# Performance work log

Hardware: AMD Instinct MI355X
Metric: run time of the kernel (lower is better)

The kernel has to match this reference:

```python
import jax, jax.numpy as jnp
import numpy as np

N = 10000
IN_F = 512
OUT_F = 64
ALPHA = 0.2
NEG_INF = -9e15


def setup_inputs() -> dict:
    key = jax.random.key(0)
    k1, k2, k3, k4, k5, k6 = jax.random.split(key, 6)
    x = jax.random.normal(k1, (N, IN_F), dtype=jnp.float32)
    adj = jax.random.randint(k2, (N, N), 0, 2).astype(jnp.float32)
    M = jax.random.uniform(k3, (N, N), dtype=jnp.float32)
    W = jax.random.normal(k4, (IN_F, OUT_F), dtype=jnp.float32) * (1.414 / np.sqrt(IN_F))
    a_self = jax.random.normal(k5, (OUT_F, 1), dtype=jnp.float32) * 0.1
    a_neighs = jax.random.normal(k6, (OUT_F, 1), dtype=jnp.float32) * 0.1
    return {"x": x, "adj": adj, "M": M, "W": W, "a_self": a_self, "a_neighs": a_neighs}


def reference(x, adj, M, W, a_self, a_neighs):
    # h: [N, out_features]
    h = x @ W
    attn_for_self = h @ a_self      # [N, 1]
    attn_for_neighs = h @ a_neighs  # [N, 1]
    # outer-sum broadcast -> [N, N]
    attn_dense = attn_for_self + attn_for_neighs.T
    attn_dense = attn_dense * M
    attn_dense = jax.nn.leaky_relu(attn_dense, negative_slope=ALPHA)
    scores = jnp.where(adj > 0, attn_dense, NEG_INF)
    attention = jax.nn.softmax(scores, axis=1)
    h_prime = attention @ h  # [N, out_features]
    return jax.nn.elu(h_prime)  # concat=True path
```

## Files before the change

### kernel.cpp

```cpp
#include <hip/hip_runtime.h>
#include <math.h>

#define Nn 10000
#define NPAD 10048
#define INF_ 512
#define OUTF 64
#define ALPHA 0.2f
#define LOG2E 1.4426950408889634f

#define TI 32
#define TJ 64
#define NTILES ((Nn + TJ - 1) / TJ)
#define YS 6
#define TPC ((NTILES + YS - 1) / YS)

typedef __attribute__((ext_vector_type(8))) short bfrag;
typedef __attribute__((ext_vector_type(4))) float facc;

#define WS_S    0
#define WS_T    (Nn)
#define WS_TMAX (2*Nn)
#define WS_DEN  (2*Nn + 16)
#define WS_HP   (WS_DEN + YS*Nn)
#define WS_HBT  (WS_HP + YS*Nn*OUTF)

__device__ __forceinline__ unsigned short f2bf(float f) {
    unsigned int u = __float_as_uint(f);
    u += 0x7fffu + ((u >> 16) & 1u);
    return (unsigned short)(u >> 16);
}
__device__ __forceinline__ unsigned int pk2(float a, float b) {
    return (unsigned int)f2bf(a) | ((unsigned int)f2bf(b) << 16);
}

__global__ __launch_bounds__(256) void hgemm_kernel(
    const float* __restrict__ x, const float* __restrict__ W,
    const float* __restrict__ a_self, const float* __restrict__ a_neighs,
    unsigned short* __restrict__ hbfT, float* __restrict__ s, float* __restrict__ t)
{
    const int col  = threadIdx.x & 63;
    const int wid  = threadIdx.x >> 6;
    const int row0 = blockIdx.x * 16 + wid * 4;
    const float* x0 = x + row0 * INF_;

    float acc0 = 0.f, acc1 = 0.f, acc2 = 0.f, acc3 = 0.f;
    #pragma unroll 4
    for (int k4 = 0; k4 < INF_ / 4; ++k4) {
        const int k = k4 << 2;
        const float w0 = W[(k    ) * OUTF + col];
        const float w1 = W[(k + 1) * OUTF + col];
        const float w2 = W[(k + 2) * OUTF + col];
        const float w3 = W[(k + 3) * OUTF + col];
        const float4 xa = *(const float4*)(x0 +          k);
        const float4 xb = *(const float4*)(x0 +   INF_ + k);
        const float4 xc = *(const float4*)(x0 + 2*INF_ + k);
        const float4 xd = *(const float4*)(x0 + 3*INF_ + k);
        acc0 = fmaf(xa.x,w0, fmaf(xa.y,w1, fmaf(xa.z,w2, fmaf(xa.w,w3, acc0))));
        acc1 = fmaf(xb.x,w0, fmaf(xb.y,w1, fmaf(xb.z,w2, fmaf(xb.w,w3, acc1))));
        acc2 = fmaf(xc.x,w0, fmaf(xc.y,w1, fmaf(xc.z,w2, fmaf(xc.w,w3, acc2))));
        acc3 = fmaf(xd.x,w0, fmaf(xd.y,w1, fmaf(xd.z,w2, fmaf(xd.w,w3, acc3))));
    }
    ushort4 hb;
    hb.x = f2bf(acc0); hb.y = f2bf(acc1); hb.z = f2bf(acc2); hb.w = f2bf(acc3);
    *(ushort4*)(hbfT + (size_t)col * NPAD + row0) = hb;

    const float as = a_self[col], an = a_neighs[col];
    #define RED(ACC, U) { \
        float vs = (ACC) * as, vn = (ACC) * an; \
        _Pragma("unroll") \
        for (int d_ = 32; d_; d_ >>= 1) { vs += __shfl_xor(vs, d_); vn += __shfl_xor(vn, d_); } \
        if (col == 0) { s[row0 + (U)] = vs; t[row0 + (U)] = vn; } }
    RED(acc0, 0) RED(acc1, 1) RED(acc2, 2) RED(acc3, 3)
    #undef RED
}

__global__ __launch_bounds__(1024) void tmax_kernel(
    const float* __restrict__ t, float* __restrict__ tmax)
{
    __shared__ float red[16];
    float m = -3e38f;
    for (int i = threadIdx.x; i < Nn; i += 1024) m = fmaxf(m, t[i]);
    #pragma unroll
    for (int d = 32; d; d >>= 1) m = fmaxf(m, __shfl_xor(m, d));
    if ((threadIdx.x & 63) == 0) red[threadIdx.x >> 6] = m;
    __syncthreads();
    if (threadIdx.x < 16) {
        m = red[threadIdx.x];
        #pragma unroll
        for (int d = 8; d; d >>= 1) m = fmaxf(m, __shfl_xor(m, d));
        if (threadIdx.x == 0) *tmax = m;
    }
}

__global__ __launch_bounds__(256, 4) void gat_main_kernel(
    const float* __restrict__ adj, const float* __restrict__ Mm,
    const unsigned short* __restrict__ hbfT, const float* __restrict__ sv,
    const float* __restrict__ tv, const float* __restrict__ tmaxp,
    float* __restrict__ den_part, float* __restrict__ hp_part)
{
    __shared__ __align__(16) unsigned short hTl[OUTF][TJ + 8];
    __shared__ __align__(16) unsigned short Pl[TI][TJ + 8];

    const int tid = threadIdx.x;
    const int i0  = blockIdx.x * TI;
    const int tlo = blockIdx.y * TPC;
    const int thi = min(NTILES, tlo + TPC);

    const int rr = tid >> 3, jc = tid & 7;
    const int prow = i0 + rr;
    const bool rowok = prow < Nn;
    const float si = rowok ? sv[prow] : 0.0f;
    const float mc = fmaxf(0.0f, si + *tmaxp) * LOG2E;
    const float* aRow = adj + (size_t)prow * Nn;
    const float* mRow = Mm  + (size_t)prow * Nn;

    const int hc_ = tid >> 2, hseg = tid & 3;
    const unsigned short* hsrc = hbfT + (size_t)hc_ * NPAD + hseg * 16;

    const int lane = tid & 63, wv = tid >> 6;
    const int l15 = lane & 15, kq = lane >> 4;
    const int rb = wv & 1, cbp = wv >> 1;
    const unsigned short* aP  = &Pl[rb * 16 + l15][kq * 8];
    const unsigned short* bP0 = &hTl[cbp * 32 + l15][kq * 8];
    const unsigned short* bP1 = bP0 + 16 * (TJ + 8);

    facc accA = {0.f, 0.f, 0.f, 0.f}, accB = {0.f, 0.f, 0.f, 0.f};
    float denacc = 0.0f;

    const float4 z4 = make_float4(0.f, 0.f, 0.f, 0.f);
    float4 pa0 = z4, pa1 = z4, pm0 = z4, pm1 = z4, pt0 = z4, pt1 = z4;
    uint4 ph0 = make_uint4(0,0,0,0), ph1 = make_uint4(0,0,0,0);

    auto prefetch = [&](int tile) {
        const int j0 = tile * TJ;
        ph0 = *(const uint4*)(hsrc + j0);
        ph1 = *(const uint4*)(hsrc + j0 + 8);
        const int jl = j0 + (jc << 3);
        if (rowok && jl + 7 < Nn) {
            pa0 = *(const float4*)(aRow + jl); pa1 = *(const float4*)(aRow + jl + 4);
            pm0 = *(const float4*)(mRow + jl); pm1 = *(const float4*)(mRow + jl + 4);
            pt0 = *(const float4*)(tv   + jl); pt1 = *(const float4*)(tv   + jl + 4);
        } else {
            pa0 = pa1 = pm0 = pm1 = pt0 = pt1 = z4;
            if (rowok) {
                #define LD1(dst, base, off) if ((jl + (off)) < Nn) dst = (base)[jl + (off)]
                LD1(pa0.x, aRow, 0); LD1(pa0.y, aRow, 1); LD1(pa0.z, aRow, 2); LD1(pa0.w, aRow, 3);
                LD1(pa1.x, aRow, 4); LD1(pa1.y, aRow, 5); LD1(pa1.z, aRow, 6); LD1(pa1.w, aRow, 7);
                LD1(pm0.x, mRow, 0); LD1(pm0.y, mRow, 1); LD1(pm0.z, mRow, 2); LD1(pm0.w, mRow, 3);
                LD1(pm1.x, mRow, 4); LD1(pm1.y, mRow, 5); LD1(pm1.z, mRow, 6); LD1(pm1.w, mRow, 7);
                LD1(pt0.x, tv,   0); LD1(pt0.y, tv,   1); LD1(pt0.z, tv,   2); LD1(pt0.w, tv,   3);
                LD1(pt1.x, tv,   4); LD1(pt1.y, tv,   5); LD1(pt1.z, tv,   6); LD1(pt1.w, tv,   7);
                #undef LD1
            }
        }
    };

    #define PC(dst, av, mv, tvv) { \
        float e_ = (si + (tvv)) * (mv); \
        float l_ = fmaxf(e_, ALPHA * e_); \
        dst = ((av) > 0.0f) ? exp2f(fmaf(l_, LOG2E, -mc)) : 0.0f; }

    prefetch(tlo);
    for (int tile = tlo; tile < thi; ++tile) {
        __syncthreads();

        *(uint4*)&hTl[hc_][hseg * 16]     = ph0;
        *(uint4*)&hTl[hc_][hseg * 16 + 8] = ph1;

        float4 p40, p41;
        PC(p40.x, pa0.x, pm0.x, pt0.x); PC(p40.y, pa0.y, pm0.y, pt0.y);
        PC(p40.z, pa0.z, pm0.z, pt0.z); PC(p40.w, pa0.w, pm0.w, pt0.w);
        PC(p41.x, pa1.x, pm1.x, pt1.x); PC(p41.y, pa1.y, pm1.y, pt1.y);
        PC(p41.z, pa1.z, pm1.z, pt1.z); PC(p41.w, pa1.w, pm1.w, pt1.w);
        denacc += ((p40.x + p40.y) + (p40.z + p40.w)) + ((p41.x + p41.y) + (p41.z + p41.w));

        uint4 pw;
        pw.x = pk2(p40.x, p40.y); pw.y = pk2(p40.z, p40.w);
        pw.z = pk2(p41.x, p41.y); pw.w = pk2(p41.z, p41.w);
        *(uint4*)&Pl[rr][jc << 3] = pw;

        __syncthreads();

        if (tile + 1 < thi) prefetch(tile + 1);
        asm volatile("" ::: "memory");

        #pragma unroll
        for (int k0 = 0; k0 < TJ; k0 += 32) {
            const bfrag af = *(const bfrag*)(aP  + k0);
            const bfrag b0 = *(const bfrag*)(bP0 + k0);
            const bfrag b1 = *(const bfrag*)(bP1 + k0);
            accA = __builtin_amdgcn_mfma_f32_16x16x32_bf16(af, b0, accA, 0, 0, 0);
            accB = __builtin_amdgcn_mfma_f32_16x16x32_bf16(af, b1, accB, 0, 0, 0);
        }
    }
    #undef PC

    float d = denacc;
    d += __shfl_xor(d, 1); d += __shfl_xor(d, 2); d += __shfl_xor(d, 4);
    if (rowok && jc == 0) den_part[blockIdx.y * Nn + prow] = d;

    float* hp = hp_part + (size_t)blockIdx.y * (Nn * OUTF);
    const int orow = i0 + rb * 16 + (kq << 2);
    const int oc   = cbp * 32 + l15;
    #pragma unroll
    for (int r = 0; r < 4; ++r) {
        if (orow + r < Nn) {
            hp[(orow + r) * OUTF + oc]      = accA[r];
            hp[(orow + r) * OUTF + oc + 16] = accB[r];
        }
    }
}

__global__ __launch_bounds__(256) void finalize_kernel(
    const float* __restrict__ dp, const float* __restrict__ hp,
    float* __restrict__ out)
{
    const int idx = blockIdx.x * 256 + threadIdx.x;
    const int S = Nn * OUTF;
    const int row = idx >> 6;
    float num = 0.0f, den = 0.0f;
    #pragma unroll
    for (int y = 0; y < YS; ++y) {
        num += hp[(size_t)y * S + idx];
        den += dp[y * Nn + row];
    }
    const float v = num / den;
    out[idx] = (v > 0.0f) ? v : expm1f(v);
}

extern "C" void kernel_launch(void* const* d_in, const int* in_sizes, int n_in,
                              void* d_out, int out_size, void* d_ws, size_t ws_size,
                              hipStream_t stream) {
    const float* x        = (const float*)d_in[0];
    const float* adj      = (const float*)d_in[1];
    const float* Mm       = (const float*)d_in[2];
    const float* W        = (const float*)d_in[3];
    const float* a_self   = (const float*)d_in[4];
    const float* a_neighs = (const float*)d_in[5];

    float* out  = (float*)d_out;
    float* ws   = (float*)d_ws;
    float* s    = ws + WS_S;
    float* t    = ws + WS_T;
    float* tmax = ws + WS_TMAX;
    float* denp = ws + WS_DEN;
    float* hpp  = ws + WS_HP;
    unsigned short* hbfT = (unsigned short*)(ws + WS_HBT);

    hgemm_kernel<<<Nn / 16, 256, 0, stream>>>(x, W, a_self, a_neighs, hbfT, s, t);
    tmax_kernel<<<1, 1024, 0, stream>>>(t, tmax);
    gat_main_kernel<<<dim3((Nn + TI - 1) / TI, YS), 256, 0, stream>>>(
        adj, Mm, hbfT, s, t, tmax, denp, hpp);
    finalize_kernel<<<(Nn * OUTF) / 256, 256, 0, stream>>>(denp, hpp, out);
}
```

Before: 266.5 us.

## Compute attention weights directly in MFMA A-fragment registers, dropping LDS staging

The main kernel is restructured so each wave owns 16 rows and each lane loads adj/M values laid out to match the MFMA A-operand fragment. Probabilities are packed to bf16 straight into registers, and the B operand (transposed bf16 h) is read directly from global/L2. This removes the shared-memory tiles, both __syncthreads per tile, and the explicit software prefetch. Adj/M loads become nontemporal and TI grows to 64, so each wave computes all 64 output columns. The trade-offs are redundant per-wave global reads of h, loss of explicit load/compute overlap, and strided 32-byte row accesses per lane.

```diff
diff --git a/kernel.cpp b/kernel.cpp
--- a/kernel.cpp
+++ b/kernel.cpp
@@ -8,14 +8,16 @@
 #define ALPHA 0.2f
 #define LOG2E 1.4426950408889634f
 
-#define TI 32
+#define TI 64
 #define TJ 64
 #define NTILES ((Nn + TJ - 1) / TJ)
+#define NIB    ((Nn + TI - 1) / TI)
 #define YS 6
 #define TPC ((NTILES + YS - 1) / YS)
 
 typedef __attribute__((ext_vector_type(8))) short bfrag;
 typedef __attribute__((ext_vector_type(4))) float facc;
+typedef __attribute__((ext_vector_type(4))) float f32x4;
 
 #define WS_S    0
 #define WS_T    (Nn)
@@ -92,121 +94,119 @@
     }
 }
 
-__global__ __launch_bounds__(256, 4) void gat_main_kernel(
+__global__ __launch_bounds__(256) void gat_main_kernel(
     const float* __restrict__ adj, const float* __restrict__ Mm,
     const unsigned short* __restrict__ hbfT, const float* __restrict__ sv,
     const float* __restrict__ tv, const float* __restrict__ tmaxp,
     float* __restrict__ den_part, float* __restrict__ hp_part)
 {
-    __shared__ __align__(16) unsigned short hTl[OUTF][TJ + 8];
-    __shared__ __align__(16) unsigned short Pl[TI][TJ + 8];
-
-    const int tid = threadIdx.x;
-    const int i0  = blockIdx.x * TI;
-    const int tlo = blockIdx.y * TPC;
-    const int thi = min(NTILES, tlo + TPC);
-
-    const int rr = tid >> 3, jc = tid & 7;
-    const int prow = i0 + rr;
-    const bool rowok = prow < Nn;
-    const float si = rowok ? sv[prow] : 0.0f;
+    const int tid  = threadIdx.x;
+    const int lane = tid & 63, wv = tid >> 6;
+    const int l15  = lane & 15, kq = lane >> 4;
+    const int i0   = blockIdx.x * TI;
+    const int tlo  = blockIdx.y * TPC;
+    const int thi  = min(NTILES, tlo + TPC);
+
+    const int  row   = i0 + wv * 16 + l15;
+    const bool rowok = row < Nn;
+    const int  rowc  = min(row, Nn - 1);
+    const float si = sv[rowc];
     const float mc = fmaxf(0.0f, si + *tmaxp) * LOG2E;
-    const float* aRow = adj + (size_t)prow * Nn;
-    const float* mRow = Mm  + (size_t)prow * Nn;
-
-    const int hc_ = tid >> 2, hseg = tid & 3;
-    const unsigned short* hsrc = hbfT + (size_t)hc_ * NPAD + hseg * 16;
-
-    const int lane = tid & 63, wv = tid >> 6;
-    const int l15 = lane & 15, kq = lane >> 4;
-    const int rb = wv & 1, cbp = wv >> 1;
-    const unsigned short* aP  = &Pl[rb * 16 + l15][kq * 8];
-    const unsigned short* bP0 = &hTl[cbp * 32 + l15][kq * 8];
-    const unsigned short* bP1 = bP0 + 16 * (TJ + 8);
-
-    facc accA = {0.f, 0.f, 0.f, 0.f}, accB = {0.f, 0.f, 0.f, 0.f};
+    const float* aRow = adj + (size_t)rowc * Nn;
+    const float* mRow = Mm  + (size_t)rowc * Nn;
+
+    const unsigned short* hB0 = hbfT + (size_t)(l15     ) * NPAD;
+    const unsigned short* hB1 = hbfT + (size_t)(l15 + 16) * NPAD;
+    const unsigned short* hB2 = hbfT + (size_t)(l15 + 32) * NPAD;
+    const unsigned short* hB3 = hbfT + (size_t)(l15 + 48) * NPAD;
+
+    facc acc0 = {0.f,0.f,0.f,0.f}, acc1 = {0.f,0.f,0.f,0.f};
+    facc acc2 = {0.f,0.f,0.f,0.f}, acc3 = {0.f,0.f,0.f,0.f};
     float denacc = 0.0f;
-
-    const float4 z4 = make_float4(0.f, 0.f, 0.f, 0.f);
-    float4 pa0 = z4, pa1 = z4, pm0 = z4, pm1 = z4, pt0 = z4, pt1 = z4;
-    uint4 ph0 = make_uint4(0,0,0,0), ph1 = make_uint4(0,0,0,0);
-
-    auto prefetch = [&](int tile) {
-        const int j0 = tile * TJ;
-        ph0 = *(const uint4*)(hsrc + j0);
-        ph1 = *(const uint4*)(hsrc + j0 + 8);
-        const int jl = j0 + (jc << 3);
-        if (rowok && jl + 7 < Nn) {
-            pa0 = *(const float4*)(aRow + jl); pa1 = *(const float4*)(aRow + jl + 4);
-            pm0 = *(const float4*)(mRow + jl); pm1 = *(const float4*)(mRow + jl + 4);
-            pt0 = *(const float4*)(tv   + jl); pt1 = *(const float4*)(tv   + jl + 4);
-        } else {
-            pa0 = pa1 = pm0 = pm1 = pt0 = pt1 = z4;
-            if (rowok) {
-                #define LD1(dst, base, off) if ((jl + (off)) < Nn) dst = (base)[jl + (off)]
-                LD1(pa0.x, aRow, 0); LD1(pa0.y, aRow, 1); LD1(pa0.z, aRow, 2); LD1(pa0.w, aRow, 3);
-                LD1(pa1.x, aRow, 4); LD1(pa1.y, aRow, 5); LD1(pa1.z, aRow, 6); LD1(pa1.w, aRow, 7);
-                LD1(pm0.x, mRow, 0); LD1(pm0.y, mRow, 1); LD1(pm0.z, mRow, 2); LD1(pm0.w, mRow, 3);
-                LD1(pm1.x, mRow, 4); LD1(pm1.y, mRow, 5); LD1(pm1.z, mRow, 6); LD1(pm1.w, mRow, 7);
-                LD1(pt0.x, tv,   0); LD1(pt0.y, tv,   1); LD1(pt0.z, tv,   2); LD1(pt0.w, tv,   3);
-                LD1(pt1.x, tv,   4); LD1(pt1.y, tv,   5); LD1(pt1.z, tv,   6); LD1(pt1.w, tv,   7);
-                #undef LD1
-            }
-        }
-    };
 
     #define PC(dst, av, mv, tvv) { \
         float e_ = (si + (tvv)) * (mv); \
         float l_ = fmaxf(e_, ALPHA * e_); \
         dst = ((av) > 0.0f) ? exp2f(fmaf(l_, LOG2E, -mc)) : 0.0f; }
 
-    prefetch(tlo);
-    for (int tile = tlo; tile < thi; ++tile) {
-        __syncthreads();
-
-        *(uint4*)&hTl[hc_][hseg * 16]     = ph0;
-        *(uint4*)&hTl[hc_][hseg * 16 + 8] = ph1;
-
-        float4 p40, p41;
-        PC(p40.x, pa0.x, pm0.x, pt0.x); PC(p40.y, pa0.y, pm0.y, pt0.y);
-        PC(p40.z, pa0.z, pm0.z, pt0.z); PC(p40.w, pa0.w, pm0.w, pt0.w);
-        PC(p41.x, pa1.x, pm1.x, pt1.x); PC(p41.y, pa1.y, pm1.y, pt1.y);
-        PC(p41.z, pa1.z, pm1.z, pt1.z); PC(p41.w, pa1.w, pm1.w, pt1.w);
-        denacc += ((p40.x + p40.y) + (p40.z + p40.w)) + ((p41.x + p41.y) + (p41.z + p41.w));
-
-        uint4 pw;
-        pw.x = pk2(p40.x, p40.y); pw.y = pk2(p40.z, p40.w);
-        pw.z = pk2(p41.x, p41.y); pw.w = pk2(p41.z, p41.w);
-        *(uint4*)&Pl[rr][jc << 3] = pw;
-
-        __syncthreads();
-
-        if (tile + 1 < thi) prefetch(tile + 1);
-        asm volatile("" ::: "memory");
-
-        #pragma unroll
-        for (int k0 = 0; k0 < TJ; k0 += 32) {
-            const bfrag af = *(const bfrag*)(aP  + k0);
-            const bfrag b0 = *(const bfrag*)(bP0 + k0);
-            const bfrag b1 = *(const bfrag*)(bP1 + k0);
-            accA = __builtin_amdgcn_mfma_f32_16x16x32_bf16(af, b0, accA, 0, 0, 0);
-            accB = __builtin_amdgcn_mfma_f32_16x16x32_bf16(af, b1, accB, 0, 0, 0);
-        }
+    for (int t = tlo; t < thi; ++t) {
+        const int j0 = t * TJ;
+        const int jA = j0 + kq * 8;
+        const int jB = jA + 32;
+        const bool okA = jA < Nn, okB = jB < Nn;
+        const int  cA  = okA ? jA : (Nn - 8);
+        const int  cB  = okB ? jB : (Nn - 8);
+
+        const f32x4 a0 = __builtin_nontemporal_load((const f32x4*)(aRow + cA));
+        const f32x4 a1 = __builtin_nontemporal_load((const f32x4*)(aRow + cA + 4));
+        const f32x4 a2 = __builtin_nontemporal_load((const f32x4*)(aRow + cB));
+        const f32x4 a3 = __builtin_nontemporal_load((const f32x4*)(aRow + cB + 4));
+        const f32x4 m0 = __builtin_nontemporal_load((const f32x4*)(mRow + cA));
+        const f32x4 m1 = __builtin_nontemporal_load((const f32x4*)(mRow + cA + 4));
+        const f32x4 m2 = __builtin_nontemporal_load((const f32x4*)(mRow + cB));
+        const f32x4 m3 = __builtin_nontemporal_load((const f32x4*)(mRow + cB + 4));
+        const f32x4 t0 = *(const f32x4*)(tv + cA);
+        const f32x4 t1 = *(const f32x4*)(tv + cA + 4);
+        const f32x4 t2 = *(const f32x4*)(tv + cB);
+        const f32x4 t3 = *(const f32x4*)(tv + cB + 4);
+
+        f32x4 p0, p1, p2, p3;
+        PC(p0.x, a0.x, m0.x, t0.x); PC(p0.y, a0.y, m0.y, t0.y);
+        PC(p0.z, a0.z, m0.z, t0.z); PC(p0.w, a0.w, m0.w, t0.w);
+        PC(p1.x, a1.x, m1.x, t1.x); PC(p1.y, a1.y, m1.y, t1.y);
+        PC(p1.z, a1.z, m1.z, t1.z); PC(p1.w, a1.w, m1.w, t1.w);
+        PC(p2.x, a2.x, m2.x, t2.x); PC(p2.y, a2.y, m2.y, t2.y);
+        PC(p2.z, a2.z, m2.z, t2.z); PC(p2.w, a2.w, m2.w, t2.w);
+        PC(p3.x, a3.x, m3.x, t3.x); PC(p3.y, a3.y, m3.y, t3.y);
+        PC(p3.z, a3.z, m3.z, t3.z); PC(p3.w, a3.w, m3.w, t3.w);
+        if (!okA) { p0 = (f32x4){0.f,0.f,0.f,0.f}; p1 = p0; }
+        if (!okB) { p2 = (f32x4){0.f,0.f,0.f,0.f}; p3 = p2; }
+
+        denacc += ((p0.x + p0.y) + (p0.z + p0.w)) + ((p1.x + p1.y) + (p1.z + p1.w))
+                + ((p2.x + p2.y) + (p2.z + p2.w)) + ((p3.x + p3.y) + (p3.z + p3.w));
+
+        uint4 awA, awB;
+        awA.x = pk2(p0.x, p0.y); awA.y = pk2(p0.z, p0.w);
+        awA.z = pk2(p1.x, p1.y); awA.w = pk2(p1.z, p1.w);
+        awB.x = pk2(p2.x, p2.y); awB.y = pk2(p2.z, p2.w);
+        awB.z = pk2(p3.x, p3.y); awB.w = pk2(p3.z, p3.w);
+        const bfrag afA = *(const bfrag*)&awA;
+        const bfrag afB = *(const bfrag*)&awB;
+
+        const bfrag b0A = *(const bfrag*)(hB0 + jA);
+        const bfrag b0B = *(const bfrag*)(hB0 + jB);
+        const bfrag b1A = *(const bfrag*)(hB1 + jA);
+        const bfrag b1B = *(const bfrag*)(hB1 + jB);
+        const bfrag b2A = *(const bfrag*)(hB2 + jA);
+        const bfrag b2B = *(const bfrag*)(hB2 + jB);
+        const bfrag b3A = *(const bfrag*)(hB3 + jA);
+        const bfrag b3B = *(const bfrag*)(hB3 + jB);
+
+        acc0 = __builtin_amdgcn_mfma_f32_16x16x32_bf16(afA, b0A, acc0, 0, 0, 0);
+        acc1 = __builtin_amdgcn_mfma_f32_16x16x32_bf16(afA, b1A, acc1, 0, 0, 0);
+        acc2 = __builtin_amdgcn_mfma_f32_16x16x32_bf16(afA, b2A, acc2, 0, 0, 0);
+        acc3 = __builtin_amdgcn_mfma_f32_16x16x32_bf16(afA, b3A, acc3, 0, 0, 0);
+        acc0 = __builtin_amdgcn_mfma_f32_16x16x32_bf16(afB, b0B, acc0, 0, 0, 0);
+        acc1 = __builtin_amdgcn_mfma_f32_16x16x32_bf16(afB, b1B, acc1, 0, 0, 0);
+        acc2 = __builtin_amdgcn_mfma_f32_16x16x32_bf16(afB, b2B, acc2, 0, 0, 0);
+        acc3 = __builtin_amdgcn_mfma_f32_16x16x32_bf16(afB, b3B, acc3, 0, 0, 0);
     }
     #undef PC
 
-    float d = denacc;
-    d += __shfl_xor(d, 1); d += __shfl_xor(d, 2); d += __shfl_xor(d, 4);
-    if (rowok && jc == 0) den_part[blockIdx.y * Nn + prow] = d;
+    denacc += __shfl_xor(denacc, 16);
+    denacc += __shfl_xor(denacc, 32);
+    if (rowok && kq == 0) den_part[blockIdx.y * Nn + row] = denacc;
 
     float* hp = hp_part + (size_t)blockIdx.y * (Nn * OUTF);
-    const int orow = i0 + rb * 16 + (kq << 2);
-    const int oc   = cbp * 32 + l15;
+    const int orow = i0 + wv * 16 + (kq << 2);
     #pragma unroll
     for (int r = 0; r < 4; ++r) {
         if (orow + r < Nn) {
-            hp[(orow + r) * OUTF + oc]      = accA[r];
-            hp[(orow + r) * OUTF + oc + 16] = accB[r];
+            float* dst = hp + (size_t)(orow + r) * OUTF + l15;
+            dst[0]  = acc0[r];
+            dst[16] = acc1[r];
+            dst[32] = acc2[r];
+            dst[48] = acc3[r];
         }
     }
 }
@@ -249,7 +249,7 @@
 
     hgemm_kernel<<<Nn / 16, 256, 0, stream>>>(x, W, a_self, a_neighs, hbfT, s, t);
     tmax_kernel<<<1, 1024, 0, stream>>>(t, tmax);
-    gat_main_kernel<<<dim3((Nn + TI - 1) / TI, YS), 256, 0, stream>>>(
+    gat_main_kernel<<<dim3(NIB, YS), 256, 0, stream>>>(
         adj, Mm, hbfT, s, t, tmax, denp, hpp);
     finalize_kernel<<<(Nn * OUTF) / 256, 256, 0, stream>>>(denp, hpp, out);
 }
```

Result: slower. 430.5 us (+61.5%).
